# Kernel optimization log

Measured on AMD Instinct MI355X. Metric: run time of the kernel, lower is better.

Reference implementation:

```python
import jax, jax.numpy as jnp
import numpy as np


def setup_inputs() -> dict:
    key = jax.random.key(0)
    ks = jax.random.split(key, 6)
    B, S, D_in, D_out = 4, 4096, 512, 64
    return {
        "inputs_for_keys": jax.random.normal(ks[0], (B, S, D_in), dtype=jnp.float32),
        "inputs_for_values": jax.random.normal(ks[1], (B, S, D_in), dtype=jnp.float32),
        "inputs_for_queries": jax.random.normal(ks[2], (B, S, D_in), dtype=jnp.float32),
        "Wk": jax.random.normal(ks[3], (D_in, D_out), dtype=jnp.float32) * 0.01,
        "Wq": jax.random.normal(ks[4], (D_in, D_out), dtype=jnp.float32) * 0.01,
        "Wv": jax.random.normal(ks[5], (D_in, D_out), dtype=jnp.float32) * 0.01,
    }


def reference(inputs_for_keys, inputs_for_values, inputs_for_queries, Wk, Wq, Wv):
    # Projections: [B, S, D_in] @ [D_in, D_out] -> [B, S, D_out]
    K = jnp.einsum("bsd,de->bse", inputs_for_keys, Wk)
    V = jnp.einsum("bsd,de->bse", inputs_for_values, Wv)
    Q = jnp.einsum("bqd,de->bqe", inputs_for_queries, Wq)

    Sq, Sk = Q.shape[1], K.shape[1]
    # NOTE: original scales by sqrt(window_size_keys), NOT sqrt(head_dim).
    scale = 1.0 / jnp.sqrt(jnp.float32(Sk))
    score = jnp.einsum("bqe,bke->bqk", Q, K) * scale  # [B, Sq, Sk]

    # Causal mask: -inf strictly above the diagonal (use_mask = is_self_attention = True)
    causal = jnp.tril(jnp.ones((Sq, Sk), dtype=bool))
    score = jnp.where(causal[None, :, :], score, -jnp.inf)

    attn = jax.nn.softmax(score, axis=-1)  # [B, Sq, Sk]
    return jnp.einsum("bqk,bke->bqe", attn, V)  # [B, Sq, D_out]
```

## Files before the change

### kernel.cpp

```cpp
#include <hip/hip_runtime.h>

#define BATCH 4
#define SEQ   4096
#define DIN   512
#define DOUT  64

typedef short bf16x8 __attribute__((ext_vector_type(8)));
typedef float f32x4  __attribute__((ext_vector_type(4)));

__device__ inline unsigned short bf16_fast(float f) {
    return (unsigned short)((__float_as_uint(f) + 0x8000u) >> 16);
}
__device__ inline unsigned int pack2(float a, float b) {
    unsigned int ua = __float_as_uint(a) + 0x8000u;
    unsigned int ub = __float_as_uint(b) + 0x8000u;
    return __builtin_amdgcn_perm(ub, ua, 0x07060302u);
}

__global__ void prep_wt(const float* __restrict__ Wk, const float* __restrict__ Wv,
                        const float* __restrict__ Wq, unsigned short* __restrict__ wt) {
    int idx = blockIdx.x * blockDim.x + threadIdx.x;
    if (idx >= 3 * DOUT * DIN) return;
    int t = idx / (DOUT * DIN);
    int rem = idx % (DOUT * DIN);
    int n = rem / DIN, k = rem % DIN;
    const float* W = (t == 0) ? Wk : (t == 1) ? Wv : Wq;
    wt[idx] = bf16_fast(W[k * DOUT + n]);
}

__global__ __launch_bounds__(256) void proj_kernel(
    const float* __restrict__ Xk, const float* __restrict__ Xv, const float* __restrict__ Xq,
    const unsigned short* __restrict__ wt,
    unsigned short* __restrict__ k_ws, unsigned short* __restrict__ vt_ws,
    unsigned short* __restrict__ q_ws)
{
    int tz = blockIdx.y;
    const float* X = (tz == 0) ? Xk : (tz == 1) ? Xv : Xq;
    const unsigned short* Wt = wt + (size_t)tz * DOUT * DIN;

    int wave = threadIdx.x >> 6;
    int lane = threadIdx.x & 63;
    int l16 = lane & 15, quad = lane >> 4;
    int m0 = blockIdx.x * 64 + wave * 16;

    f32x4 acc[4] = {{0.f,0.f,0.f,0.f},{0.f,0.f,0.f,0.f},{0.f,0.f,0.f,0.f},{0.f,0.f,0.f,0.f}};
    const float* xrow = X + (size_t)(m0 + l16) * DIN + quad * 8;

    #pragma unroll 4
    for (int kk = 0; kk < DIN; kk += 32) {
        float4 xa = *(const float4*)(xrow + kk);
        float4 xb = *(const float4*)(xrow + kk + 4);
        union { unsigned int u[4]; bf16x8 v; } xf;
        xf.u[0] = pack2(xa.x, xa.y);
        xf.u[1] = pack2(xa.z, xa.w);
        xf.u[2] = pack2(xb.x, xb.y);
        xf.u[3] = pack2(xb.z, xb.w);
        #pragma unroll
        for (int i = 0; i < 4; i++) {
            bf16x8 wf = *(const bf16x8*)(Wt + (size_t)(16 * i + l16) * DIN + kk + quad * 8);
            acc[i] = __builtin_amdgcn_mfma_f32_16x16x32_bf16(wf, xf.v, acc[i], 0, 0, 0);
        }
    }

    int grow = m0 + l16;
    if (tz == 1) {
        int bb = grow >> 12, s = grow & 4095;
        #pragma unroll
        for (int i = 0; i < 4; i++)
            #pragma unroll
            for (int r = 0; r < 4; r++) {
                int d = 16 * i + quad * 4 + r;
                vt_ws[(((size_t)(bb * DOUT + d)) << 12) + s] = bf16_fast(acc[i][r]);
            }
    } else {
        unsigned short* outp = (tz == 0) ? k_ws : q_ws;
        #pragma unroll
        for (int i = 0; i < 4; i++) {
            uint2 st;
            st.x = pack2(acc[i][0], acc[i][1]);
            st.y = pack2(acc[i][2], acc[i][3]);
            *(uint2*)(outp + (size_t)grow * DOUT + 16 * i + quad * 4) = st;
        }
    }
}

__global__ __launch_bounds__(256) void attn_partial(
    const unsigned short* __restrict__ q_ws,
    const unsigned short* __restrict__ k_ws,
    const unsigned short* __restrict__ vt_ws,
    float* __restrict__ po, float* __restrict__ pml)
{
    int bid = blockIdx.x;
    int t = 63 - (bid >> 4);
    int rem = bid & 15;
    int b = rem >> 2;
    int c = rem & 3;

    int niter = t + 1 - 16 * c;
    if (niter <= 0) return;
    if (niter > 16) niter = 16;
    bool has_diag = ((t >> 4) == c);

    __shared__ __align__(16) unsigned short Kl[64 * 72];
    __shared__ __align__(16) unsigned short Vl[64 * 72];
    __shared__ __align__(16) unsigned short Pl[4 * 16 * 72];

    int wave = threadIdx.x >> 6, lane = threadIdx.x & 63;
    int l16 = lane & 15, quad = lane >> 4;
    int q0 = t * 64 + wave * 16;

    const unsigned short* qrow = q_ws + ((size_t)(b * SEQ + q0 + l16)) * DOUT + quad * 8;
    bf16x8 qf0 = *(const bf16x8*)(qrow);
    bf16x8 qf1 = *(const bf16x8*)(qrow + 32);

    f32x4 o[4] = {{0.f,0.f,0.f,0.f},{0.f,0.f,0.f,0.f},{0.f,0.f,0.f,0.f},{0.f,0.f,0.f,0.f}};
    float lp[4] = {0.f, 0.f, 0.f, 0.f};

    const float C2 = 0.0225421100f;

    for (int it = 0; it < niter; it++) {
        int k0 = (c * 16 + it) * 64;
        __syncthreads();
        #pragma unroll
        for (int ch = threadIdx.x; ch < 512; ch += 256) {
            int row = ch >> 3, off = ch & 7;
            *(uint4*)&Kl[row * 72 + off * 8] =
                *(const uint4*)(k_ws + ((size_t)(b * SEQ + k0 + row)) * DOUT + off * 8);
            *(uint4*)&Vl[row * 72 + off * 8] =
                *(const uint4*)(vt_ws + (((size_t)(b * DOUT + row)) << 12) + k0 + off * 8);
        }
        __syncthreads();

        f32x4 s[4];
        #pragma unroll
        for (int i = 0; i < 4; i++) {
            bf16x8 kf0 = *(const bf16x8*)&Kl[(16 * i + l16) * 72 + quad * 8];
            bf16x8 kf1 = *(const bf16x8*)&Kl[(16 * i + l16) * 72 + 32 + quad * 8];
            f32x4 z = {0.f, 0.f, 0.f, 0.f};
            z = __builtin_amdgcn_mfma_f32_16x16x32_bf16(qf0, kf0, z, 0, 0, 0);
            s[i] = __builtin_amdgcn_mfma_f32_16x16x32_bf16(qf1, kf1, z, 0, 0, 0);
        }

        unsigned short* pw = &Pl[wave * 16 * 72];
        bool diag = has_diag && (it == niter - 1);
        #pragma unroll
        for (int r = 0; r < 4; r++) {
            int qr = q0 + quad * 4 + r;
            #pragma unroll
            for (int i = 0; i < 4; i++) {
                int kg = k0 + 16 * i + l16;
                float p = exp2f(s[i][r] * C2);
                if (diag && kg > qr) p = 0.f;
                lp[r] += p;
                pw[(quad * 4 + r) * 72 + 16 * i + l16] = bf16_fast(p);
            }
        }

        bf16x8 pf0 = *(const bf16x8*)&pw[l16 * 72 + quad * 8];
        bf16x8 pf1 = *(const bf16x8*)&pw[l16 * 72 + 32 + quad * 8];
        #pragma unroll
        for (int i = 0; i < 4; i++) {
            bf16x8 vf0 = *(const bf16x8*)&Vl[(16 * i + l16) * 72 + quad * 8];
            bf16x8 vf1 = *(const bf16x8*)&Vl[(16 * i + l16) * 72 + 32 + quad * 8];
            o[i] = __builtin_amdgcn_mfma_f32_16x16x32_bf16(pf0, vf0, o[i], 0, 0, 0);
            o[i] = __builtin_amdgcn_mfma_f32_16x16x32_bf16(pf1, vf1, o[i], 0, 0, 0);
        }
    }

    #pragma unroll
    for (int r = 0; r < 4; r++) {
        lp[r] += __shfl_xor(lp[r], 1);
        lp[r] += __shfl_xor(lp[r], 2);
        lp[r] += __shfl_xor(lp[r], 4);
        lp[r] += __shfl_xor(lp[r], 8);
    }

    int u = (b * 64 + t) * 4 + c;
    float* pOu = po + (size_t)u * 4096 + (size_t)(wave * 16) * 64;
    #pragma unroll
    for (int i = 0; i < 4; i++)
        #pragma unroll
        for (int r = 0; r < 4; r++)
            pOu[(quad * 4 + r) * 64 + 16 * i + l16] = o[i][r];

    if (l16 == 0) {
        float* pm = pml + (size_t)u * 64 + wave * 16 + quad * 4;
        #pragma unroll
        for (int r = 0; r < 4; r++) pm[r] = lp[r];
    }
}

__global__ __launch_bounds__(256) void attn_combine(
    const float* __restrict__ po, const float* __restrict__ pml,
    float* __restrict__ out)
{
    int unit = blockIdx.x >> 1, half = blockIdx.x & 1;
    int b = unit >> 6, t = unit & 63;
    int nch = (t >> 4) + 1;
    int tid = threadIdx.x;
    int row = half * 32 + (tid >> 3);
    int col0 = (tid & 7) * 8;

    float lsum = 0.f;
    float acc[8] = {0.f,0.f,0.f,0.f,0.f,0.f,0.f,0.f};
    for (int c = 0; c < nch; c++) {
        int u = unit * 4 + c;
        lsum += pml[(size_t)u * 64 + row];
        const float* Oc = po + (size_t)u * 4096 + row * 64 + col0;
        float4 a = *(const float4*)(Oc);
        float4 bv = *(const float4*)(Oc + 4);
        acc[0] += a.x; acc[1] += a.y; acc[2] += a.z; acc[3] += a.w;
        acc[4] += bv.x; acc[5] += bv.y; acc[6] += bv.z; acc[7] += bv.w;
    }
    float inv = 1.0f / lsum;
    float* op = out + ((size_t)(b * SEQ + t * 64 + row)) * DOUT + col0;
    #pragma unroll
    for (int j = 0; j < 8; j++) op[j] = acc[j] * inv;
}

extern "C" void kernel_launch(void* const* d_in, const int* in_sizes, int n_in,
                              void* d_out, int out_size, void* d_ws, size_t ws_size,
                              hipStream_t stream) {
    const float* Xk = (const float*)d_in[0];
    const float* Xv = (const float*)d_in[1];
    const float* Xq = (const float*)d_in[2];
    const float* Wk = (const float*)d_in[3];
    const float* Wq = (const float*)d_in[4];
    const float* Wv = (const float*)d_in[5];
    float* out = (float*)d_out;

    unsigned short* ws = (unsigned short*)d_ws;
    const size_t NE = (size_t)BATCH * SEQ * DOUT;
    unsigned short* k_ws  = ws;
    unsigned short* vt_ws = ws + NE;
    unsigned short* q_ws  = ws + 2 * NE;
    unsigned short* wt_ws = ws + 3 * NE;
    float* pf  = (float*)(ws + 3 * NE + 3 * DOUT * DIN);
    float* po  = pf;
    float* pml = pf + (size_t)1024 * 4096;

    prep_wt<<<(3 * DOUT * DIN + 255) / 256, 256, 0, stream>>>(Wk, Wv, Wq, wt_ws);
    proj_kernel<<<dim3((BATCH * SEQ) / 64, 3), 256, 0, stream>>>(Xk, Xv, Xq, wt_ws,
                                                                 k_ws, vt_ws, q_ws);
    attn_partial<<<1024, 256, 0, stream>>>(q_ws, k_ws, vt_ws, po, pml);
    attn_combine<<<512, 256, 0, stream>>>(po, pml, out);
}
```

Baseline: 191.7 us.

## Load K/V fragments directly from global memory and make each wave an independent query tile

Drops the shared-memory K/V staging and both block-wide barriers per iteration; each wave now reads its K and V^T MFMA fragments straight from global memory (relying on L1/L2 for reuse across the four waves). It also swaps the MFMA operand order so the transposed score layout lets each lane own one query row, which turns the row-sum reduction into two shuffles and allows packed bf16 stores of P. Partial outputs are now indexed per 16-row tile and written as float4, and the combine kernel is regridded to match. The trade-off is more global/cache traffic for K/V in exchange for no LDS copies or barriers and a higher occupancy hint.

```diff
diff --git a/kernel.cpp b/kernel.cpp
--- a/kernel.cpp
+++ b/kernel.cpp
@@ -84,136 +84,126 @@
     }
 }
 
-__global__ __launch_bounds__(256) void attn_partial(
+__global__ __launch_bounds__(256, 4) void attn_partial(
     const unsigned short* __restrict__ q_ws,
     const unsigned short* __restrict__ k_ws,
     const unsigned short* __restrict__ vt_ws,
     float* __restrict__ po, float* __restrict__ pml)
 {
     int bid = blockIdx.x;
-    int t = 63 - (bid >> 4);
+    int t64 = 63 - (bid >> 4);
     int rem = bid & 15;
     int b = rem >> 2;
     int c = rem & 3;
 
-    int niter = t + 1 - 16 * c;
+    int niter = t64 - 16 * c + 1;
     if (niter <= 0) return;
     if (niter > 16) niter = 16;
-    bool has_diag = ((t >> 4) == c);
-
-    __shared__ __align__(16) unsigned short Kl[64 * 72];
-    __shared__ __align__(16) unsigned short Vl[64 * 72];
+    bool has_diag = ((t64 >> 4) == c);
+
     __shared__ __align__(16) unsigned short Pl[4 * 16 * 72];
 
     int wave = threadIdx.x >> 6, lane = threadIdx.x & 63;
     int l16 = lane & 15, quad = lane >> 4;
-    int q0 = t * 64 + wave * 16;
+    int t16 = t64 * 4 + wave;
+    int q0 = t16 * 16;
 
     const unsigned short* qrow = q_ws + ((size_t)(b * SEQ + q0 + l16)) * DOUT + quad * 8;
     bf16x8 qf0 = *(const bf16x8*)(qrow);
     bf16x8 qf1 = *(const bf16x8*)(qrow + 32);
 
+    const unsigned short* kbase = k_ws + (size_t)b * SEQ * DOUT;
+    const unsigned short* vbase = vt_ws + (size_t)b * DOUT * SEQ;
+    unsigned short* pw = &Pl[wave * 16 * 72];
+
     f32x4 o[4] = {{0.f,0.f,0.f,0.f},{0.f,0.f,0.f,0.f},{0.f,0.f,0.f,0.f},{0.f,0.f,0.f,0.f}};
-    float lp[4] = {0.f, 0.f, 0.f, 0.f};
-
-    const float C2 = 0.0225421100f;
+    float lp = 0.f;
+    const float C2 = 0.02254211f;
 
     for (int it = 0; it < niter; it++) {
-        int k0 = (c * 16 + it) * 64;
-        __syncthreads();
-        #pragma unroll
-        for (int ch = threadIdx.x; ch < 512; ch += 256) {
-            int row = ch >> 3, off = ch & 7;
-            *(uint4*)&Kl[row * 72 + off * 8] =
-                *(const uint4*)(k_ws + ((size_t)(b * SEQ + k0 + row)) * DOUT + off * 8);
-            *(uint4*)&Vl[row * 72 + off * 8] =
-                *(const uint4*)(vt_ws + (((size_t)(b * DOUT + row)) << 12) + k0 + off * 8);
-        }
-        __syncthreads();
+        int k0 = c * 1024 + it * 64;
 
         f32x4 s[4];
         #pragma unroll
         for (int i = 0; i < 4; i++) {
-            bf16x8 kf0 = *(const bf16x8*)&Kl[(16 * i + l16) * 72 + quad * 8];
-            bf16x8 kf1 = *(const bf16x8*)&Kl[(16 * i + l16) * 72 + 32 + quad * 8];
+            const unsigned short* kr = kbase + (size_t)(k0 + 16 * i + l16) * DOUT + quad * 8;
+            bf16x8 ka = *(const bf16x8*)kr;
+            bf16x8 kb = *(const bf16x8*)(kr + 32);
             f32x4 z = {0.f, 0.f, 0.f, 0.f};
-            z = __builtin_amdgcn_mfma_f32_16x16x32_bf16(qf0, kf0, z, 0, 0, 0);
-            s[i] = __builtin_amdgcn_mfma_f32_16x16x32_bf16(qf1, kf1, z, 0, 0, 0);
-        }
-
-        unsigned short* pw = &Pl[wave * 16 * 72];
+            z    = __builtin_amdgcn_mfma_f32_16x16x32_bf16(ka, qf0, z, 0, 0, 0);
+            s[i] = __builtin_amdgcn_mfma_f32_16x16x32_bf16(kb, qf1, z, 0, 0, 0);
+        }
+
         bool diag = has_diag && (it == niter - 1);
-        #pragma unroll
-        for (int r = 0; r < 4; r++) {
-            int qr = q0 + quad * 4 + r;
-            #pragma unroll
-            for (int i = 0; i < 4; i++) {
-                int kg = k0 + 16 * i + l16;
-                float p = exp2f(s[i][r] * C2);
-                if (diag && kg > qr) p = 0.f;
-                lp[r] += p;
-                pw[(quad * 4 + r) * 72 + 16 * i + l16] = bf16_fast(p);
+        int qg = q0 + l16;
+        #pragma unroll
+        for (int i = 0; i < 4; i++) {
+            int kg = k0 + 16 * i + quad * 4;
+            float p0 = exp2f(s[i][0] * C2);
+            float p1 = exp2f(s[i][1] * C2);
+            float p2 = exp2f(s[i][2] * C2);
+            float p3 = exp2f(s[i][3] * C2);
+            if (diag) {
+                if (kg + 0 > qg) p0 = 0.f;
+                if (kg + 1 > qg) p1 = 0.f;
+                if (kg + 2 > qg) p2 = 0.f;
+                if (kg + 3 > qg) p3 = 0.f;
             }
+            lp += (p0 + p1) + (p2 + p3);
+            *(unsigned int*)&pw[l16 * 72 + 16 * i + quad * 4]     = pack2(p0, p1);
+            *(unsigned int*)&pw[l16 * 72 + 16 * i + quad * 4 + 2] = pack2(p2, p3);
         }
 
         bf16x8 pf0 = *(const bf16x8*)&pw[l16 * 72 + quad * 8];
         bf16x8 pf1 = *(const bf16x8*)&pw[l16 * 72 + 32 + quad * 8];
-        #pragma unroll
-        for (int i = 0; i < 4; i++) {
-            bf16x8 vf0 = *(const bf16x8*)&Vl[(16 * i + l16) * 72 + quad * 8];
-            bf16x8 vf1 = *(const bf16x8*)&Vl[(16 * i + l16) * 72 + 32 + quad * 8];
-            o[i] = __builtin_amdgcn_mfma_f32_16x16x32_bf16(pf0, vf0, o[i], 0, 0, 0);
-            o[i] = __builtin_amdgcn_mfma_f32_16x16x32_bf16(pf1, vf1, o[i], 0, 0, 0);
-        }
-    }
-
+
+        #pragma unroll
+        for (int i = 0; i < 4; i++) {
+            const unsigned short* vr = vbase + (size_t)(16 * i + l16) * SEQ + k0 + quad * 8;
+            bf16x8 va = *(const bf16x8*)vr;
+            bf16x8 vb = *(const bf16x8*)(vr + 32);
+            o[i] = __builtin_amdgcn_mfma_f32_16x16x32_bf16(va, pf0, o[i], 0, 0, 0);
+            o[i] = __builtin_amdgcn_mfma_f32_16x16x32_bf16(vb, pf1, o[i], 0, 0, 0);
+        }
+    }
+
+    lp += __shfl_xor(lp, 16);
+    lp += __shfl_xor(lp, 32);
+
+    int u = (b * 256 + t16) * 4 + c;
+    float* pOu = po + (size_t)u * 1024;
     #pragma unroll
-    for (int r = 0; r < 4; r++) {
-        lp[r] += __shfl_xor(lp[r], 1);
-        lp[r] += __shfl_xor(lp[r], 2);
-        lp[r] += __shfl_xor(lp[r], 4);
-        lp[r] += __shfl_xor(lp[r], 8);
-    }
-
-    int u = (b * 64 + t) * 4 + c;
-    float* pOu = po + (size_t)u * 4096 + (size_t)(wave * 16) * 64;
-    #pragma unroll
-    for (int i = 0; i < 4; i++)
-        #pragma unroll
-        for (int r = 0; r < 4; r++)
-            pOu[(quad * 4 + r) * 64 + 16 * i + l16] = o[i][r];
-
-    if (l16 == 0) {
-        float* pm = pml + (size_t)u * 64 + wave * 16 + quad * 4;
-        #pragma unroll
-        for (int r = 0; r < 4; r++) pm[r] = lp[r];
-    }
-}
-
-__global__ __launch_bounds__(256) void attn_combine(
+    for (int i = 0; i < 4; i++) {
+        float4 st = {o[i][0], o[i][1], o[i][2], o[i][3]};
+        *(float4*)&pOu[l16 * 64 + 16 * i + quad * 4] = st;
+    }
+    if (lane < 16) pml[(size_t)u * 16 + l16] = lp;
+}
+
+__global__ __launch_bounds__(128) void attn_combine(
     const float* __restrict__ po, const float* __restrict__ pml,
     float* __restrict__ out)
 {
-    int unit = blockIdx.x >> 1, half = blockIdx.x & 1;
-    int b = unit >> 6, t = unit & 63;
-    int nch = (t >> 4) + 1;
+    int unit = blockIdx.x;
+    int b = unit >> 8, t16 = unit & 255;
+    int nch = (t16 >> 6) + 1;
     int tid = threadIdx.x;
-    int row = half * 32 + (tid >> 3);
+    int row = tid >> 3;
     int col0 = (tid & 7) * 8;
 
     float lsum = 0.f;
     float acc[8] = {0.f,0.f,0.f,0.f,0.f,0.f,0.f,0.f};
     for (int c = 0; c < nch; c++) {
         int u = unit * 4 + c;
-        lsum += pml[(size_t)u * 64 + row];
-        const float* Oc = po + (size_t)u * 4096 + row * 64 + col0;
+        lsum += pml[(size_t)u * 16 + row];
+        const float* Oc = po + (size_t)u * 1024 + row * 64 + col0;
         float4 a = *(const float4*)(Oc);
         float4 bv = *(const float4*)(Oc + 4);
         acc[0] += a.x; acc[1] += a.y; acc[2] += a.z; acc[3] += a.w;
         acc[4] += bv.x; acc[5] += bv.y; acc[6] += bv.z; acc[7] += bv.w;
     }
     float inv = 1.0f / lsum;
-    float* op = out + ((size_t)(b * SEQ + t * 64 + row)) * DOUT + col0;
+    float* op = out + ((size_t)(b * SEQ + t16 * 16 + row)) * DOUT + col0;
     #pragma unroll
     for (int j = 0; j < 8; j++) op[j] = acc[j] * inv;
 }
@@ -237,11 +227,11 @@
     unsigned short* wt_ws = ws + 3 * NE;
     float* pf  = (float*)(ws + 3 * NE + 3 * DOUT * DIN);
     float* po  = pf;
-    float* pml = pf + (size_t)1024 * 4096;
+    float* pml = pf + (size_t)4096 * 1024;
 
     prep_wt<<<(3 * DOUT * DIN + 255) / 256, 256, 0, stream>>>(Wk, Wv, Wq, wt_ws);
     proj_kernel<<<dim3((BATCH * SEQ) / 64, 3), 256, 0, stream>>>(Xk, Xv, Xq, wt_ws,
                                                                  k_ws, vt_ws, q_ws);
     attn_partial<<<1024, 256, 0, stream>>>(q_ws, k_ws, vt_ws, po, pml);
-    attn_combine<<<512, 256, 0, stream>>>(po, pml, out);
-}
+    attn_combine<<<1024, 128, 0, stream>>>(po, pml, out);
+}
```

After: 264.3 us. 1.38x slower.
